# Performance work log

Measured on AMD Instinct MI355X. Metric: run time of the kernel, lower is better.

The kernel has to match this reference:

```python
import jax, jax.numpy as jnp
import numpy as np

S, B, C, H, E = 4096, 2, 256, 8, 131072
CC = C // H


def setup_inputs() -> dict:
    key = jax.random.key(0)
    ks = jax.random.split(key, 12)
    sc = 0.02
    inp = {
        "x": jax.random.normal(ks[0], (S, B, C), jnp.float32),
        "q_id": jax.random.randint(ks[1], (E,), 0, S, jnp.int32),
        "k_id": jax.random.randint(ks[2], (E,), 0, S, jnp.int32),
        "Wq": jax.random.normal(ks[3], (C, C), jnp.float32) * sc,
        "bq": jnp.zeros((C,), jnp.float32),
        "Wk": jax.random.normal(ks[4], (C, C), jnp.float32) * sc,
        "bk": jnp.zeros((C,), jnp.float32),
        "Wv": jax.random.normal(ks[5], (C, C), jnp.float32) * sc,
        "bv": jnp.zeros((C,), jnp.float32),
        "Wx": jax.random.normal(ks[6], (C, C), jnp.float32) * sc,
        "bx": jnp.zeros((C,), jnp.float32),
    }
    return inp


def reference(x, q_id, k_id, Wq, bq, Wk, bk, Wv, bv, Wx, bx):
    s, b, c = x.shape
    cc = c // H
    # qkv projections (torch Linear: x @ W.T + b)
    q = (x @ Wq.T + bq).reshape(s, b, H, cc)
    k = (x @ Wk.T + bk).reshape(s, b, H, cc)
    v = (x @ Wv.T + bv).reshape(s, b, H, cc)
    # per-edge scores: gather along sequence axis by edge ids
    qk = jnp.einsum('ebhc,ebhc->ebh', q[q_id], k[k_id])[..., None]  # [E,b,h,1]
    qk = qk / jnp.sqrt(jnp.asarray(cc, x.dtype))
    eqk = jnp.exp(qk - jnp.max(qk))  # global max, as in original
    # scatter-add softmax normalizer and weighted sum over edges
    d = jnp.zeros((s, b, H, 1), x.dtype).at[q_id].add(eqk)
    out = jnp.zeros((s, b, H, cc), x.dtype).at[q_id].add(eqk * v[k_id])
    out = (out / d).reshape(s, b, c)
    return out @ Wx.T + bx
```

## Files before the change

kernel.cpp:

```cpp
#include <hip/hip_runtime.h>

constexpr int S_  = 4096;
constexpr int B_  = 2;
constexpr int C_  = 256;
constexpr int H_  = 8;
constexpr int E_  = 131072;
constexpr int CC_ = 32;
constexpr int MR  = S_ * B_;

typedef __attribute__((ext_vector_type(8))) short bf16x8_t;
typedef __attribute__((ext_vector_type(4))) float f32x4_t;

__device__ __forceinline__ unsigned short f2bf(float f) {
    unsigned int u = __float_as_uint(f);
    u += 0x7fffu + ((u >> 16) & 1u);
    return (unsigned short)(u >> 16);
}
__device__ __forceinline__ float bflo(unsigned int u) { return __uint_as_float(u << 16); }
__device__ __forceinline__ float bfhi(unsigned int u) { return __uint_as_float(u & 0xffff0000u); }


__global__ void hist_kernel(const int* __restrict__ q_id, int* __restrict__ count) {
    int e = blockIdx.x * 256 + threadIdx.x;
    atomicAdd(&count[q_id[e]], 1);
}

__global__ __launch_bounds__(1024) void scan_kernel(const int* __restrict__ count,
                                                    int* __restrict__ base,
                                                    int* __restrict__ cursor) {
    __shared__ int sums[1024];
    int t = threadIdx.x;
    int c0 = count[4 * t + 0], c1 = count[4 * t + 1];
    int c2 = count[4 * t + 2], c3 = count[4 * t + 3];
    int tsum = c0 + c1 + c2 + c3;
    sums[t] = tsum;
    __syncthreads();
    for (int off = 1; off < 1024; off <<= 1) {
        int val = (t >= off) ? sums[t - off] : 0;
        __syncthreads();
        sums[t] += val;
        __syncthreads();
    }
    int excl = sums[t] - tsum;
    int b0 = excl, b1 = b0 + c0, b2 = b1 + c1, b3 = b2 + c2;
    base[4 * t + 0] = b0; base[4 * t + 1] = b1;
    base[4 * t + 2] = b2; base[4 * t + 3] = b3;
    cursor[4 * t + 0] = b0; cursor[4 * t + 1] = b1;
    cursor[4 * t + 2] = b2; cursor[4 * t + 3] = b3;
    if (t == 1023) base[S_] = b3 + c3;
}

__global__ void scatter_kernel(const int* __restrict__ q_id, const int* __restrict__ k_id,
                               int* __restrict__ cursor, int* __restrict__ kid_sorted) {
    int e = blockIdx.x * 256 + threadIdx.x;
    int pos = atomicAdd(&cursor[q_id[e]], 1);
    kid_sorted[pos] = k_id[e];
}


__global__ void cast_x_kernel(const float* __restrict__ src, unsigned short* __restrict__ dst) {
    int i = blockIdx.x * 256 + threadIdx.x;
    const float4* s = (const float4*)src + (size_t)i * 2;
    float4 a = s[0], b = s[1];
    uint4 o;
    o.x = (unsigned)f2bf(a.x) | ((unsigned)f2bf(a.y) << 16);
    o.y = (unsigned)f2bf(a.z) | ((unsigned)f2bf(a.w) << 16);
    o.z = (unsigned)f2bf(b.x) | ((unsigned)f2bf(b.y) << 16);
    o.w = (unsigned)f2bf(b.z) | ((unsigned)f2bf(b.w) << 16);
    *((uint4*)dst + i) = o;
}

__global__ void cast_w4_kernel(const float* __restrict__ Wq, const float* __restrict__ Wk,
                               const float* __restrict__ Wv, const float* __restrict__ Wx,
                               unsigned short* __restrict__ dst) {
    int z = blockIdx.z;
    const float* src = (z == 0) ? Wq : (z == 1) ? Wk : (z == 2) ? Wv : Wx;
    unsigned short* d = dst + (size_t)z * (C_ * C_);
    int i = blockIdx.x * 256 + threadIdx.x;
    const float4* s = (const float4*)src + (size_t)i * 2;
    float4 a = s[0], b = s[1];
    uint4 o;
    o.x = (unsigned)f2bf(a.x) | ((unsigned)f2bf(a.y) << 16);
    o.y = (unsigned)f2bf(a.z) | ((unsigned)f2bf(a.w) << 16);
    o.z = (unsigned)f2bf(b.x) | ((unsigned)f2bf(b.y) << 16);
    o.w = (unsigned)f2bf(b.z) | ((unsigned)f2bf(b.w) << 16);
    *((uint4*)d + i) = o;
}


__device__ __forceinline__ void gemm_mfma_body(
        const unsigned short* __restrict__ A, const unsigned short* __restrict__ W,
        const float* __restrict__ bias,
        unsigned short* __restrict__ outb, float* __restrict__ outf,
        int ostride, int ooff, int bm, int bn) {
    __shared__ __align__(16) unsigned short As[128][72];
    __shared__ __align__(16) unsigned short Bs[128][72];
    const int tid = threadIdx.x;
    const int lane = tid & 63, wave = tid >> 6;
    const int wm = wave >> 1, wn = wave & 1;
    const int l16 = lane & 15, quad = lane >> 4;
    f32x4_t acc[4][4] = {};

    for (int k0 = 0; k0 < C_; k0 += 64) {
#pragma unroll
        for (int i = 0; i < 4; ++i) {
            int l = i * 256 + tid;
            int r = l >> 3, c8 = (l & 7) << 3;
            *(uint4*)&As[r][c8] = *(const uint4*)&A[(size_t)(bm + r) * C_ + k0 + c8];
            *(uint4*)&Bs[r][c8] = *(const uint4*)&W[(size_t)(bn + r) * C_ + k0 + c8];
        }
        __syncthreads();
#pragma unroll
        for (int ks = 0; ks < 2; ++ks) {
            bf16x8_t af[4], bf[4];
#pragma unroll
            for (int t = 0; t < 4; ++t)
                af[t] = *(const bf16x8_t*)&As[wm * 64 + t * 16 + l16][ks * 32 + quad * 8];
#pragma unroll
            for (int t = 0; t < 4; ++t)
                bf[t] = *(const bf16x8_t*)&Bs[wn * 64 + t * 16 + l16][ks * 32 + quad * 8];
#pragma unroll
            for (int i = 0; i < 4; ++i)
#pragma unroll
                for (int j = 0; j < 4; ++j)
                    acc[i][j] = __builtin_amdgcn_mfma_f32_16x16x32_bf16(af[i], bf[j], acc[i][j], 0, 0, 0);
        }
        __syncthreads();
    }
#pragma unroll
    for (int tn = 0; tn < 4; ++tn) {
        const int col = bn + wn * 64 + tn * 16 + l16;
        const float bv = bias[col];
#pragma unroll
        for (int tm = 0; tm < 4; ++tm) {
            const int row0 = bm + wm * 64 + tm * 16 + quad * 4;
#pragma unroll
            for (int r = 0; r < 4; ++r) {
                float val = acc[tm][tn][r] + bv;
                if (outb) outb[(size_t)(row0 + r) * ostride + ooff + col] = f2bf(val);
                else      outf[(size_t)(row0 + r) * C_ + col] = val;
            }
        }
    }
}

__global__ __launch_bounds__(256) void gemm_qkv(
        const unsigned short* __restrict__ xb, const unsigned short* __restrict__ Wb,
        const float* __restrict__ bq, const float* __restrict__ bk, const float* __restrict__ bv,
        unsigned short* __restrict__ qb, unsigned short* __restrict__ kvb) {
    int z = blockIdx.z;
    const unsigned short* W = Wb + (size_t)z * (C_ * C_);
    const float* bias = (z == 0) ? bq : (z == 1) ? bk : bv;
    unsigned short* outb = (z == 0) ? qb : kvb;
    int stride = (z == 0) ? 256 : 512;
    int off = (z == 2) ? 256 : 0;
    gemm_mfma_body(xb, W, bias, outb, nullptr, stride, off, blockIdx.x * 128, blockIdx.y * 128);
}

__global__ __launch_bounds__(256) void gemm_proj(
        const unsigned short* __restrict__ attnb, const unsigned short* __restrict__ Wxb,
        const float* __restrict__ bx, float* __restrict__ out) {
    gemm_mfma_body(attnb, Wxb, bx, nullptr, out, 0, 0, blockIdx.x * 128, blockIdx.y * 128);
}


__global__ __launch_bounds__(256) void attn_edge(
        const unsigned short* __restrict__ qb, const unsigned short* __restrict__ kvb,
        const int* __restrict__ base, const int* __restrict__ kid,
        unsigned short* __restrict__ attnb) {
    const int lane = threadIdx.x & 63;
    const int wave = threadIdx.x >> 6;
    const int s = blockIdx.x * 4 + wave;
    const int half = lane >> 5, hl = lane & 31;
    const int e0 = __builtin_amdgcn_readfirstlane(base[s]);
    const int e1 = __builtin_amdgcn_readfirstlane(base[s + 1]);

    const uint4 qq = *((const uint4*)(qb + (size_t)(s * 2 + half) * C_) + hl);
    const float q0 = bflo(qq.x), q1 = bfhi(qq.x), q2 = bflo(qq.y), q3 = bfhi(qq.y);
    const float q4 = bflo(qq.z), q5 = bfhi(qq.z), q6 = bflo(qq.w), q7 = bfhi(qq.w);

    float a0 = 0.f, a1 = 0.f, a2 = 0.f, a3 = 0.f, a4 = 0.f, a5 = 0.f, a6 = 0.f, a7 = 0.f;
    float wsum = 0.f;
    const float scale = 0.17677669529663687f;

    for (int j = e0; j < e1; ++j) {
        const int ke = kid[j];
        const uint4* kvp = (const uint4*)(kvb + (size_t)(ke * 2 + half) * 512);
        const uint4 kk = kvp[hl];
        const uint4 vv = kvp[32 + hl];
        float p = q0 * bflo(kk.x) + q1 * bfhi(kk.x)
                + q2 * bflo(kk.y) + q3 * bfhi(kk.y)
                + q4 * bflo(kk.z) + q5 * bfhi(kk.z)
                + q6 * bflo(kk.w) + q7 * bfhi(kk.w);
        p += __shfl_xor(p, 1);
        p += __shfl_xor(p, 2);
        const float w = __expf(p * scale);
        a0 = fmaf(w, bflo(vv.x), a0); a1 = fmaf(w, bfhi(vv.x), a1);
        a2 = fmaf(w, bflo(vv.y), a2); a3 = fmaf(w, bfhi(vv.y), a3);
        a4 = fmaf(w, bflo(vv.z), a4); a5 = fmaf(w, bfhi(vv.z), a5);
        a6 = fmaf(w, bflo(vv.w), a6); a7 = fmaf(w, bfhi(vv.w), a7);
        wsum += w;
    }
    const float inv = 1.0f / wsum;
    uint4 o;
    o.x = (unsigned)f2bf(a0 * inv) | ((unsigned)f2bf(a1 * inv) << 16);
    o.y = (unsigned)f2bf(a2 * inv) | ((unsigned)f2bf(a3 * inv) << 16);
    o.z = (unsigned)f2bf(a4 * inv) | ((unsigned)f2bf(a5 * inv) << 16);
    o.w = (unsigned)f2bf(a6 * inv) | ((unsigned)f2bf(a7 * inv) << 16);
    *((uint4*)(attnb + (size_t)(s * 2 + half) * C_) + hl) = o;
}


extern "C" void kernel_launch(void* const* d_in, const int* in_sizes, int n_in,
                              void* d_out, int out_size, void* d_ws, size_t ws_size,
                              hipStream_t stream) {
    const float* x  = (const float*)d_in[0];
    const int* q_id = (const int*)d_in[1];
    const int* k_id = (const int*)d_in[2];
    const float* Wq = (const float*)d_in[3];
    const float* bq = (const float*)d_in[4];
    const float* Wk = (const float*)d_in[5];
    const float* bk = (const float*)d_in[6];
    const float* Wv = (const float*)d_in[7];
    const float* bv = (const float*)d_in[8];
    const float* Wx = (const float*)d_in[9];
    const float* bx = (const float*)d_in[10];
    float* out = (float*)d_out;

    char* ws = (char*)d_ws;
    unsigned short* xb    = (unsigned short*)ws;                 ws += (size_t)MR * C_ * 2;
    unsigned short* qb    = (unsigned short*)ws;                 ws += (size_t)MR * C_ * 2;
    unsigned short* kvb   = (unsigned short*)ws;                 ws += (size_t)MR * 512 * 2;
    unsigned short* attnb = (unsigned short*)ws;                 ws += (size_t)MR * C_ * 2;
    unsigned short* Wb    = (unsigned short*)ws;                 ws += (size_t)4 * C_ * C_ * 2;
    int* count      = (int*)ws;                                  ws += S_ * 4;
    int* base       = (int*)ws;                                  ws += (S_ + 1) * 4;
    int* cursor     = (int*)ws;                                  ws += S_ * 4;
    int* kid_sorted = (int*)ws;

    hipMemsetAsync(count, 0, S_ * sizeof(int), stream);
    hist_kernel<<<E_ / 256, 256, 0, stream>>>(q_id, count);
    scan_kernel<<<1, 1024, 0, stream>>>(count, base, cursor);
    scatter_kernel<<<E_ / 256, 256, 0, stream>>>(q_id, k_id, cursor, kid_sorted);

    cast_x_kernel<<<(MR * C_ / 8) / 256, 256, 0, stream>>>(x, xb);
    cast_w4_kernel<<<dim3((C_ * C_ / 8) / 256, 1, 4), 256, 0, stream>>>(Wq, Wk, Wv, Wx, Wb);

    gemm_qkv<<<dim3(MR / 128, C_ / 128, 3), 256, 0, stream>>>(xb, Wb, bq, bk, bv, qb, kvb);

    attn_edge<<<S_ / 4, 256, 0, stream>>>(qb, kvb, base, kid_sorted, attnb);

    gemm_proj<<<dim3(MR / 128, C_ / 128), 256, 0, stream>>>(attnb, Wb + (size_t)3 * C_ * C_, bx, out);
}
```

Measured before the change: 163.1 us.

## Fuse prep kernels, split attention edges across waves, stage GEMM epilogue via LDS

```diff
diff --git a/kernel.cpp b/kernel.cpp
--- a/kernel.cpp
+++ b/kernel.cpp
@@ -19,47 +19,7 @@
 __device__ __forceinline__ float bflo(unsigned int u) { return __uint_as_float(u << 16); }
 __device__ __forceinline__ float bfhi(unsigned int u) { return __uint_as_float(u & 0xffff0000u); }
 
-
-__global__ void hist_kernel(const int* __restrict__ q_id, int* __restrict__ count) {
-    int e = blockIdx.x * 256 + threadIdx.x;
-    atomicAdd(&count[q_id[e]], 1);
-}
-
-__global__ __launch_bounds__(1024) void scan_kernel(const int* __restrict__ count,
-                                                    int* __restrict__ base,
-                                                    int* __restrict__ cursor) {
-    __shared__ int sums[1024];
-    int t = threadIdx.x;
-    int c0 = count[4 * t + 0], c1 = count[4 * t + 1];
-    int c2 = count[4 * t + 2], c3 = count[4 * t + 3];
-    int tsum = c0 + c1 + c2 + c3;
-    sums[t] = tsum;
-    __syncthreads();
-    for (int off = 1; off < 1024; off <<= 1) {
-        int val = (t >= off) ? sums[t - off] : 0;
-        __syncthreads();
-        sums[t] += val;
-        __syncthreads();
-    }
-    int excl = sums[t] - tsum;
-    int b0 = excl, b1 = b0 + c0, b2 = b1 + c1, b3 = b2 + c2;
-    base[4 * t + 0] = b0; base[4 * t + 1] = b1;
-    base[4 * t + 2] = b2; base[4 * t + 3] = b3;
-    cursor[4 * t + 0] = b0; cursor[4 * t + 1] = b1;
-    cursor[4 * t + 2] = b2; cursor[4 * t + 3] = b3;
-    if (t == 1023) base[S_] = b3 + c3;
-}
-
-__global__ void scatter_kernel(const int* __restrict__ q_id, const int* __restrict__ k_id,
-                               int* __restrict__ cursor, int* __restrict__ kid_sorted) {
-    int e = blockIdx.x * 256 + threadIdx.x;
-    int pos = atomicAdd(&cursor[q_id[e]], 1);
-    kid_sorted[pos] = k_id[e];
-}
-
-
-__global__ void cast_x_kernel(const float* __restrict__ src, unsigned short* __restrict__ dst) {
-    int i = blockIdx.x * 256 + threadIdx.x;
+__device__ __forceinline__ void cast8(const float* __restrict__ src, unsigned short* __restrict__ dst, int i) {
     const float4* s = (const float4*)src + (size_t)i * 2;
     float4 a = s[0], b = s[1];
     uint4 o;
@@ -70,36 +30,73 @@
     *((uint4*)dst + i) = o;
 }
 
-__global__ void cast_w4_kernel(const float* __restrict__ Wq, const float* __restrict__ Wk,
-                               const float* __restrict__ Wv, const float* __restrict__ Wx,
-                               unsigned short* __restrict__ dst) {
-    int z = blockIdx.z;
-    const float* src = (z == 0) ? Wq : (z == 1) ? Wk : (z == 2) ? Wv : Wx;
-    unsigned short* d = dst + (size_t)z * (C_ * C_);
-    int i = blockIdx.x * 256 + threadIdx.x;
-    const float4* s = (const float4*)src + (size_t)i * 2;
-    float4 a = s[0], b = s[1];
-    uint4 o;
-    o.x = (unsigned)f2bf(a.x) | ((unsigned)f2bf(a.y) << 16);
-    o.y = (unsigned)f2bf(a.z) | ((unsigned)f2bf(a.w) << 16);
-    o.z = (unsigned)f2bf(b.x) | ((unsigned)f2bf(b.y) << 16);
-    o.w = (unsigned)f2bf(b.z) | ((unsigned)f2bf(b.w) << 16);
-    *((uint4*)d + i) = o;
-}
-
-
-__device__ __forceinline__ void gemm_mfma_body(
+
+__global__ __launch_bounds__(256) void prep_kernel(
+        const int* __restrict__ q_id, int* __restrict__ count,
+        const float* __restrict__ x, unsigned short* __restrict__ xb,
+        const float* __restrict__ Wq, const float* __restrict__ Wk,
+        const float* __restrict__ Wv, const float* __restrict__ Wx,
+        unsigned short* __restrict__ Wb) {
+    const int bid = blockIdx.x, tid = threadIdx.x;
+    if (bid < 512) {
+        atomicAdd(&count[q_id[bid * 256 + tid]], 1);
+    } else if (bid < 1536) {
+        cast8(x, xb, (bid - 512) * 256 + tid);
+    } else {
+        int idx = bid - 1536;
+        int z = idx >> 5;
+        const float* src = (z == 0) ? Wq : (z == 1) ? Wk : (z == 2) ? Wv : Wx;
+        cast8(src, Wb + (size_t)z * (C_ * C_), (idx & 31) * 256 + tid);
+    }
+}
+
+
+__global__ __launch_bounds__(1024) void scan_kernel(const int* __restrict__ count,
+                                                    int* __restrict__ base,
+                                                    int* __restrict__ cursor) {
+    __shared__ int wsums[16];
+    const int t = threadIdx.x, lane = t & 63, w = t >> 6;
+    int c0 = count[4 * t + 0], c1 = count[4 * t + 1];
+    int c2 = count[4 * t + 2], c3 = count[4 * t + 3];
+    int tsum = c0 + c1 + c2 + c3;
+    int x = tsum;
+#pragma unroll
+    for (int off = 1; off < 64; off <<= 1) {
+        int y = __shfl_up(x, off);
+        if (lane >= off) x += y;
+    }
+    if (lane == 63) wsums[w] = x;
+    __syncthreads();
+    if (t == 0) {
+        int run = 0;
+#pragma unroll
+        for (int i = 0; i < 16; ++i) { int v = wsums[i]; wsums[i] = run; run += v; }
+        base[S_] = run;
+    }
+    __syncthreads();
+    int excl = x - tsum + wsums[w];
+    int b0 = excl, b1 = b0 + c0, b2 = b1 + c1, b3 = b2 + c2;
+    base[4 * t + 0] = b0; base[4 * t + 1] = b1;
+    base[4 * t + 2] = b2; base[4 * t + 3] = b3;
+    cursor[4 * t + 0] = b0; cursor[4 * t + 1] = b1;
+    cursor[4 * t + 2] = b2; cursor[4 * t + 3] = b3;
+}
+
+
+template <int NB, bool BF16OUT>
+__device__ __forceinline__ void gemm_body(
         const unsigned short* __restrict__ A, const unsigned short* __restrict__ W,
         const float* __restrict__ bias,
         unsigned short* __restrict__ outb, float* __restrict__ outf,
         int ostride, int ooff, int bm, int bn) {
+    constexpr int NT = NB / 32;
     __shared__ __align__(16) unsigned short As[128][72];
-    __shared__ __align__(16) unsigned short Bs[128][72];
+    __shared__ __align__(16) unsigned short Bs[NB][72];
     const int tid = threadIdx.x;
     const int lane = tid & 63, wave = tid >> 6;
     const int wm = wave >> 1, wn = wave & 1;
     const int l16 = lane & 15, quad = lane >> 4;
-    f32x4_t acc[4][4] = {};
+    f32x4_t acc[4][NT] = {};
 
     for (int k0 = 0; k0 < C_; k0 += 64) {
 #pragma unroll
@@ -107,70 +104,103 @@
             int l = i * 256 + tid;
             int r = l >> 3, c8 = (l & 7) << 3;
             *(uint4*)&As[r][c8] = *(const uint4*)&A[(size_t)(bm + r) * C_ + k0 + c8];
+        }
+#pragma unroll
+        for (int i = 0; i < NT; ++i) {
+            int l = i * 256 + tid;
+            int r = l >> 3, c8 = (l & 7) << 3;
             *(uint4*)&Bs[r][c8] = *(const uint4*)&W[(size_t)(bn + r) * C_ + k0 + c8];
         }
         __syncthreads();
 #pragma unroll
         for (int ks = 0; ks < 2; ++ks) {
-            bf16x8_t af[4], bf[4];
+            bf16x8_t af[4], bf[NT];
 #pragma unroll
             for (int t = 0; t < 4; ++t)
                 af[t] = *(const bf16x8_t*)&As[wm * 64 + t * 16 + l16][ks * 32 + quad * 8];
 #pragma unroll
-            for (int t = 0; t < 4; ++t)
-                bf[t] = *(const bf16x8_t*)&Bs[wn * 64 + t * 16 + l16][ks * 32 + quad * 8];
+            for (int t = 0; t < NT; ++t)
+                bf[t] = *(const bf16x8_t*)&Bs[wn * (NB / 2) + t * 16 + l16][ks * 32 + quad * 8];
 #pragma unroll
             for (int i = 0; i < 4; ++i)
 #pragma unroll
-                for (int j = 0; j < 4; ++j)
+                for (int j = 0; j < NT; ++j)
                     acc[i][j] = __builtin_amdgcn_mfma_f32_16x16x32_bf16(af[i], bf[j], acc[i][j], 0, 0, 0);
         }
         __syncthreads();
     }
-#pragma unroll
-    for (int tn = 0; tn < 4; ++tn) {
-        const int col = bn + wn * 64 + tn * 16 + l16;
-        const float bv = bias[col];
-#pragma unroll
-        for (int tm = 0; tm < 4; ++tm) {
-            const int row0 = bm + wm * 64 + tm * 16 + quad * 4;
+
+    float bcol[NT];
+#pragma unroll
+    for (int tn = 0; tn < NT; ++tn)
+        bcol[tn] = bias[bn + wn * (NB / 2) + tn * 16 + l16];
+
+    char* buf = (char*)&As[0][0];
+#pragma unroll
+    for (int tm = 0; tm < 4; ++tm) {
+        __syncthreads();
+        const int lrow = wm * 16 + quad * 4;
+#pragma unroll
+        for (int tn = 0; tn < NT; ++tn) {
+            const int col = wn * (NB / 2) + tn * 16 + l16;
 #pragma unroll
             for (int r = 0; r < 4; ++r) {
-                float val = acc[tm][tn][r] + bv;
-                if (outb) outb[(size_t)(row0 + r) * ostride + ooff + col] = f2bf(val);
-                else      outf[(size_t)(row0 + r) * C_ + col] = val;
+                float val = acc[tm][tn][r] + bcol[tn];
+                if (BF16OUT) ((unsigned short*)(buf + (size_t)(lrow + r) * 272))[col] = f2bf(val);
+                else         ((float*)(buf + (size_t)(lrow + r) * 272))[col] = val;
             }
         }
-    }
-}
-
-__global__ __launch_bounds__(256) void gemm_qkv(
+        __syncthreads();
+#pragma unroll
+        for (int i = 0; i < 2; ++i) {
+            int f = tid * 2 + i;
+            int lr = f >> 4, cc = f & 15;
+            int grow = bm + (lr >> 4) * 64 + tm * 16 + (lr & 15);
+            if (BF16OUT)
+                *(uint4*)&outb[(size_t)grow * ostride + ooff + bn + cc * 8] =
+                    *(const uint4*)(buf + (size_t)lr * 272 + cc * 16);
+            else
+                *(float4*)&outf[(size_t)grow * C_ + bn + cc * 4] =
+                    *(const float4*)(buf + (size_t)lr * 272 + cc * 16);
+        }
+    }
+}
+
+
+__global__ __launch_bounds__(256) void scatter_qkv_kernel(
+        const int* __restrict__ q_id, const int* __restrict__ k_id,
+        int* __restrict__ cursor, int* __restrict__ koff_sorted,
         const unsigned short* __restrict__ xb, const unsigned short* __restrict__ Wb,
         const float* __restrict__ bq, const float* __restrict__ bk, const float* __restrict__ bv,
         unsigned short* __restrict__ qb, unsigned short* __restrict__ kvb) {
-    int z = blockIdx.z;
+    const int bid = blockIdx.x;
+    if (bid < 512) {
+        int e = bid * 256 + threadIdx.x;
+        int pos = atomicAdd(&cursor[q_id[e]], 1);
+        koff_sorted[pos] = k_id[e] << 10;
+        return;
+    }
+    int gb = bid - 512;
+    int z = gb >> 7, rem = gb & 127;
+    int bm = (rem >> 1) * 128, bn = (rem & 1) * 128;
     const unsigned short* W = Wb + (size_t)z * (C_ * C_);
     const float* bias = (z == 0) ? bq : (z == 1) ? bk : bv;
     unsigned short* outb = (z == 0) ? qb : kvb;
     int stride = (z == 0) ? 256 : 512;
     int off = (z == 2) ? 256 : 0;
-    gemm_mfma_body(xb, W, bias, outb, nullptr, stride, off, blockIdx.x * 128, blockIdx.y * 128);
-}
-
-__global__ __launch_bounds__(256) void gemm_proj(
-        const unsigned short* __restrict__ attnb, const unsigned short* __restrict__ Wxb,
-        const float* __restrict__ bx, float* __restrict__ out) {
-    gemm_mfma_body(attnb, Wxb, bx, nullptr, out, 0, 0, blockIdx.x * 128, blockIdx.y * 128);
+    gemm_body<128, true>(xb, W, bias, outb, nullptr, stride, off, bm, bn);
 }
 
 
 __global__ __launch_bounds__(256) void attn_edge(
         const unsigned short* __restrict__ qb, const unsigned short* __restrict__ kvb,
-        const int* __restrict__ base, const int* __restrict__ kid,
+        const int* __restrict__ base, const int* __restrict__ koff,
         unsigned short* __restrict__ attnb) {
+    __shared__ float red[2][64][9];
     const int lane = threadIdx.x & 63;
     const int wave = threadIdx.x >> 6;
-    const int s = blockIdx.x * 4 + wave;
+    const int rw = wave >> 1, part = wave & 1;
+    const int s = blockIdx.x * 2 + rw;
     const int half = lane >> 5, hl = lane & 31;
     const int e0 = __builtin_amdgcn_readfirstlane(base[s]);
     const int e1 = __builtin_amdgcn_readfirstlane(base[s + 1]);
@@ -183,9 +213,9 @@
     float wsum = 0.f;
     const float scale = 0.17677669529663687f;
 
-    for (int j = e0; j < e1; ++j) {
-        const int ke = kid[j];
-        const uint4* kvp = (const uint4*)(kvb + (size_t)(ke * 2 + half) * 512);
+    for (int j = e0 + part; j < e1; j += 2) {
+        const int kb = koff[j];
+        const uint4* kvp = (const uint4*)(kvb + kb + half * 512);
         const uint4 kk = kvp[hl];
         const uint4 vv = kvp[32 + hl];
         float p = q0 * bflo(kk.x) + q1 * bfhi(kk.x)
@@ -201,13 +231,32 @@
         a6 = fmaf(w, bflo(vv.w), a6); a7 = fmaf(w, bfhi(vv.w), a7);
         wsum += w;
     }
-    const float inv = 1.0f / wsum;
-    uint4 o;
-    o.x = (unsigned)f2bf(a0 * inv) | ((unsigned)f2bf(a1 * inv) << 16);
-    o.y = (unsigned)f2bf(a2 * inv) | ((unsigned)f2bf(a3 * inv) << 16);
-    o.z = (unsigned)f2bf(a4 * inv) | ((unsigned)f2bf(a5 * inv) << 16);
-    o.w = (unsigned)f2bf(a6 * inv) | ((unsigned)f2bf(a7 * inv) << 16);
-    *((uint4*)(attnb + (size_t)(s * 2 + half) * C_) + hl) = o;
+
+    if (part == 1) {
+        float* r = red[rw][lane];
+        r[0] = a0; r[1] = a1; r[2] = a2; r[3] = a3;
+        r[4] = a4; r[5] = a5; r[6] = a6; r[7] = a7; r[8] = wsum;
+    }
+    __syncthreads();
+    if (part == 0) {
+        const float* r = red[rw][lane];
+        a0 += r[0]; a1 += r[1]; a2 += r[2]; a3 += r[3];
+        a4 += r[4]; a5 += r[5]; a6 += r[6]; a7 += r[7]; wsum += r[8];
+        const float inv = 1.0f / wsum;
+        uint4 o;
+        o.x = (unsigned)f2bf(a0 * inv) | ((unsigned)f2bf(a1 * inv) << 16);
+        o.y = (unsigned)f2bf(a2 * inv) | ((unsigned)f2bf(a3 * inv) << 16);
+        o.z = (unsigned)f2bf(a4 * inv) | ((unsigned)f2bf(a5 * inv) << 16);
+        o.w = (unsigned)f2bf(a6 * inv) | ((unsigned)f2bf(a7 * inv) << 16);
+        *((uint4*)(attnb + (size_t)(s * 2 + half) * C_) + hl) = o;
+    }
+}
+
+
+__global__ __launch_bounds__(256) void gemm_proj(
+        const unsigned short* __restrict__ attnb, const unsigned short* __restrict__ Wxb,
+        const float* __restrict__ bx, float* __restrict__ out) {
+    gemm_body<64, false>(attnb, Wxb, bx, nullptr, out, 0, 0, blockIdx.x * 128, blockIdx.y * 64);
 }
 
 
@@ -233,22 +282,17 @@
     unsigned short* kvb   = (unsigned short*)ws;                 ws += (size_t)MR * 512 * 2;
     unsigned short* attnb = (unsigned short*)ws;                 ws += (size_t)MR * C_ * 2;
     unsigned short* Wb    = (unsigned short*)ws;                 ws += (size_t)4 * C_ * C_ * 2;
-    int* count      = (int*)ws;                                  ws += S_ * 4;
-    int* base       = (int*)ws;                                  ws += (S_ + 1) * 4;
-    int* cursor     = (int*)ws;                                  ws += S_ * 4;
-    int* kid_sorted = (int*)ws;
+    int* count       = (int*)ws;                                 ws += S_ * 4;
+    int* base        = (int*)ws;                                 ws += (S_ + 1) * 4;
+    int* cursor      = (int*)ws;                                 ws += S_ * 4;
+    int* koff_sorted = (int*)ws;
 
     hipMemsetAsync(count, 0, S_ * sizeof(int), stream);
-    hist_kernel<<<E_ / 256, 256, 0, stream>>>(q_id, count);
+    prep_kernel<<<1664, 256, 0, stream>>>(q_id, count, x, xb, Wq, Wk, Wv, Wx, Wb);
     scan_kernel<<<1, 1024, 0, stream>>>(count, base, cursor);
-    scatter_kernel<<<E_ / 256, 256, 0, stream>>>(q_id, k_id, cursor, kid_sorted);
-
-    cast_x_kernel<<<(MR * C_ / 8) / 256, 256, 0, stream>>>(x, xb);
-    cast_w4_kernel<<<dim3((C_ * C_ / 8) / 256, 1, 4), 256, 0, stream>>>(Wq, Wk, Wv, Wx, Wb);
-
-    gemm_qkv<<<dim3(MR / 128, C_ / 128, 3), 256, 0, stream>>>(xb, Wb, bq, bk, bv, qb, kvb);
-
-    attn_edge<<<S_ / 4, 256, 0, stream>>>(qb, kvb, base, kid_sorted, attnb);
-
-    gemm_proj<<<dim3(MR / 128, C_ / 128), 256, 0, stream>>>(attnb, Wb + (size_t)3 * C_ * C_, bx, out);
-}
+    scatter_qkv_kernel<<<896, 256, 0, stream>>>(q_id, k_id, cursor, koff_sorted,
+                                                xb, Wb, bq, bk, bv, qb, kvb);
+    attn_edge<<<S_ / 2, 256, 0, stream>>>(qb, kvb, base, koff_sorted, attnb);
+    gemm_proj<<<dim3(MR / 128, C_ / 64), 256, 0, stream>>>(
+        attnb, Wb + (size_t)3 * C_ * C_, bx, out);
+}
```

Measured after the change: 157.2 us. 1.04x faster.
